# Optimization experiments

Hardware: AMD Instinct MI355X
Metric: run time of the kernel (lower is better)

The kernel has to match this reference:

```python
import jax, jax.numpy as jnp
import numpy as np

N_NODES = 100000
N_EDGES = 3200000
N_GRAPHS = 256
HIDDEN = 64
F_IN = 9
GRAPH_INPUTS = 4


def setup_inputs() -> dict:
    key = jax.random.key(0)
    ks = jax.random.split(key, 20)
    x = jax.random.normal(ks[0], (N_NODES, F_IN), dtype=jnp.float32)
    edge_index = jax.random.randint(ks[1], (2, N_EDGES), 0, N_NODES)
    batch = jnp.sort(jax.random.randint(ks[2], (N_NODES,), 0, N_GRAPHS))
    batch = batch.at[0].set(0).at[-1].set(N_GRAPHS - 1)
    u = jax.random.normal(ks[3], (N_GRAPHS, GRAPH_INPUTS), dtype=jnp.float32)

    def lin(k, fi, fo):
        k1, k2 = jax.random.split(k)
        s = 1.0 / np.sqrt(fi)
        W = jax.random.uniform(k1, (fi, fo), minval=-s, maxval=s, dtype=jnp.float32)
        b = jax.random.uniform(k2, (fo,), minval=-s, maxval=s, dtype=jnp.float32)
        return W, b

    W1, b1 = lin(ks[4], F_IN, HIDDEN)
    W2, b2 = lin(ks[5], HIDDEN, HIDDEN)
    W3, b3 = lin(ks[6], HIDDEN, HIDDEN)
    A1, c1 = lin(ks[7], HIDDEN + GRAPH_INPUTS, 50)
    A2, c2 = lin(ks[8], 50, 30)
    A3, c3 = lin(ks[9], 30, 20)
    A4, c4 = lin(ks[10], 20, 5)
    A5, c5 = lin(ks[11], 5, 1)
    return dict(x=x, edge_index=edge_index, batch=batch, u=u,
                W1=W1, b1=b1, W2=W2, b2=b2, W3=W3, b3=b3,
                A1=A1, c1=c1, A2=A2, c2=c2, A3=A3, c3=c3,
                A4=A4, c4=c4, A5=A5, c5=c5)


def reference(x, edge_index, batch, u,
              W1, b1, W2, b2, W3, b3,
              A1, c1, A2, c2, A3, c3, A4, c4, A5, c5):
    N = x.shape[0]
    loops = jnp.arange(N, dtype=edge_index.dtype)
    src = jnp.concatenate([edge_index[0], loops])  # self-loops appended (PyG GCNConv default)
    dst = jnp.concatenate([edge_index[1], loops])
    deg = jax.ops.segment_sum(jnp.ones_like(dst, dtype=x.dtype), dst, num_segments=N)
    dinv = jax.lax.rsqrt(jnp.maximum(deg, 1.0))  # deg >= 1 due to self-loops
    norm = dinv[src] * dinv[dst]  # symmetric normalization

    def conv(h, W, b):
        h = h @ W
        msg = h[src] * norm[:, None]          # gather + scale
        return jax.ops.segment_sum(msg, dst, num_segments=N) + b  # scatter-add

    h = jax.nn.relu(conv(x, W1, b1))
    h = jax.nn.relu(conv(h, W2, b2))
    h = jax.nn.relu(conv(h, W3, b3))

    G = u.shape[0]
    sums = jax.ops.segment_sum(h, batch, num_segments=G)
    cnt = jax.ops.segment_sum(jnp.ones((N,), x.dtype), batch, num_segments=G)
    pooled = sums / jnp.maximum(cnt, 1.0)[:, None]  # global_mean_pool
    # dropout p=0.2 is identity at inference (training=False)
    z = jnp.concatenate([pooled, u], axis=1)
    z = jax.nn.relu(z @ A1 + c1)
    z = jax.nn.relu(z @ A2 + c2)
    z = jax.nn.relu(z @ A3 + c3)
    z = jax.nn.relu(z @ A4 + c4)
    z = jax.nn.relu(z @ A5 + c5)
    return z
```

## Files before the change

kernel.cpp:

```cpp
#include <hip/hip_runtime.h>

#define H 64
#define BNODE_SHIFT 8
#define BNODES 256
#define CHUNK 4096
#define EPT 16

static __device__ __forceinline__ float b2f(ushort b) {
    return __uint_as_float(((unsigned int)b) << 16);
}
static __device__ __forceinline__ ushort f2b(float f) {
    unsigned int u = __float_as_uint(f);
    return (ushort)((u + 0x7FFF + ((u >> 16) & 1)) >> 16);
}

__global__ void zero_i32(int* p, int n) {
    int i = blockIdx.x * blockDim.x + threadIdx.x;
    if (i < n) p[i] = 0;
}

__global__ void bucket_hist(const int* __restrict__ dst, int E,
                            int* __restrict__ bcounts, int nbuck) {
    __shared__ int hist[512];
    for (int i = threadIdx.x; i < nbuck; i += blockDim.x) hist[i] = 0;
    __syncthreads();
    for (int e = blockIdx.x * blockDim.x + threadIdx.x; e < E; e += gridDim.x * blockDim.x)
        atomicAdd(&hist[dst[e] >> BNODE_SHIFT], 1);
    __syncthreads();
    for (int i = threadIdx.x; i < nbuck; i += blockDim.x) {
        int v = hist[i];
        if (v) atomicAdd(&bcounts[i], v);
    }
}

__global__ void bucket_scan(const int* __restrict__ bcounts, int* __restrict__ boff,
                            int* __restrict__ bcur, int* __restrict__ rowstart,
                            int nbuck, int E, int N) {
    __shared__ int t[1024];
    int tid = threadIdx.x;
    int v = (tid < nbuck) ? bcounts[tid] : 0;
    t[tid] = v;
    __syncthreads();
    for (int off = 1; off < 1024; off <<= 1) {
        int x = (tid >= off) ? t[tid - off] : 0;
        __syncthreads();
        t[tid] += x;
        __syncthreads();
    }
    if (tid < nbuck) {
        int o = t[tid] - v;
        boff[tid] = o;
        bcur[tid * 16] = o;
    }
    if (tid == 0) { boff[nbuck] = E; rowstart[N] = E; }
}

__global__ void edge_sort_scatter(const int* __restrict__ src, const int* __restrict__ dst,
                                  int E, int nbuck,
                                  int* __restrict__ bcur, int* __restrict__ pairs4) {
    __shared__ int hist[392];
    __shared__ int bstart[393];
    __shared__ int cur[392];
    __shared__ int gbase[392];
    __shared__ int wsum[256];
    __shared__ int packed[CHUNK];
    __shared__ int gpos[CHUNK];

    int t = threadIdx.x;
    int chunkBase = blockIdx.x * CHUNK;

    for (int i = t; i < nbuck; i += 256) hist[i] = 0;
    __syncthreads();
#pragma unroll
    for (int k = 0; k < EPT; ++k) {
        int e = chunkBase + t + k * 256;
        if (e < E) atomicAdd(&hist[dst[e] >> BNODE_SHIFT], 1);
    }
    __syncthreads();

    int a0 = (2 * t < nbuck) ? hist[2 * t] : 0;
    int a1 = (2 * t + 1 < nbuck) ? hist[2 * t + 1] : 0;
    int s2 = a0 + a1;
    wsum[t] = s2;
    __syncthreads();
    for (int off = 1; off < 256; off <<= 1) {
        int x = (t >= off) ? wsum[t - off] : 0;
        __syncthreads();
        wsum[t] += x;
        __syncthreads();
    }
    int base = wsum[t] - s2;
    if (2 * t < nbuck)     bstart[2 * t] = base;
    if (2 * t + 1 < nbuck) bstart[2 * t + 1] = base + a0;
    if (t == 255) bstart[nbuck] = wsum[255];
    __syncthreads();

    for (int b = t; b < nbuck; b += 256) {
        int cnt = bstart[b + 1] - bstart[b];
        gbase[b] = cnt ? (atomicAdd(&bcur[b * 16], cnt) - bstart[b]) : 0;
        cur[b] = bstart[b];
    }
    __syncthreads();

    #pragma unroll
    for (int k = 0; k < EPT; ++k) {
        int e = chunkBase + t + k * 256;
        if (e < E) {
            int d = dst[e];
            int b = d >> BNODE_SHIFT;
            int pos = atomicAdd(&cur[b], 1);
            packed[pos] = src[e] | ((d & (BNODES - 1)) << 20);
            gpos[pos] = gbase[b] + pos;
        }
    }
    __syncthreads();

    int nloc = bstart[nbuck];
    for (int j = t; j < nloc; j += 256)
        pairs4[gpos[j]] = packed[j];
}

__global__ void bucket_build(const int* __restrict__ pairs4, const int* __restrict__ boff,
                             int* __restrict__ col, int* __restrict__ rowstart,
                             float* __restrict__ dinv, int N) {
    __shared__ int hist[BNODES];
    __shared__ int cur[BNODES];
    int b = blockIdx.x;
    int lo = boff[b], hi = boff[b + 1];
    int node0 = b << BNODE_SHIFT;
    int tid = threadIdx.x;
    hist[tid] = 0;
    __syncthreads();
    for (int e = lo + tid; e < hi; e += 256)
        atomicAdd(&hist[(pairs4[e] >> 20) & (BNODES - 1)], 1);
    __syncthreads();
    int v = hist[tid];
    cur[tid] = v;
    __syncthreads();
    for (int off = 1; off < BNODES; off <<= 1) {
        int x = (tid >= off) ? cur[tid - off] : 0;
        __syncthreads();
        cur[tid] += x;
        __syncthreads();
    }
    {
        int ex = cur[tid] - v;
        int node = node0 + tid;
        if (node < N) {
            rowstart[node] = lo + ex;
            dinv[node] = rsqrtf((float)(v + 1));
        }
        cur[tid] = ex;
    }
    __syncthreads();
    for (int e = lo + tid; e < hi; e += 256) {
        int pr = pairs4[e];
        int p = atomicAdd(&cur[(pr >> 20) & (BNODES - 1)], 1);
        col[lo + p] = pr & 0xFFFFF;
    }
}

__global__ void graph_bounds(const int* __restrict__ batch, int* __restrict__ nodestart,
                             int N, int G) {
    int i = blockIdx.x * blockDim.x + threadIdx.x;
    if (i >= N) return;
    int b = batch[i];
    int bp = (i == 0) ? -1 : batch[i - 1];
    for (int g = bp + 1; g <= b; ++g) nodestart[g] = i;
    if (i == N - 1) nodestart[G] = N;
}

__global__ void pool_mean(const float* __restrict__ h, const int* __restrict__ nodestart,
                          float* __restrict__ pooled, int G) {
    int g = blockIdx.x;
    int lo = nodestart[g], hi = nodestart[g + 1];
    int f = threadIdx.x & 63, w = threadIdx.x >> 6;
    float acc = 0.f;
    for (int n = lo + w; n < hi; n += 4) acc += h[(size_t)n * H + f];
    __shared__ float red[4][64];
    red[w][f] = acc;
    __syncthreads();
    if (w == 0) {
        float s = red[0][f] + red[1][f] + red[2][f] + red[3][f];
        float c = (float)(hi - lo);
        pooled[g * H + f] = s / fmaxf(c, 1.f);
    }
}

__global__ void prep_xb(const float* __restrict__ x, const float* __restrict__ dinv,
                        ushort* __restrict__ xb, int N) {
    int i = blockIdx.x * blockDim.x + threadIdx.x;
    if (i >= N * 16) return;
    int n = i >> 4, k = i & 15;
    xb[i] = (k < 9) ? f2b(x[n * 9 + k] * dinv[n]) : (ushort)0;
}

__global__ void conv1_fused(const ushort* __restrict__ xb, const float* __restrict__ dinv,
                            const int* __restrict__ rowstart,
                            const int* __restrict__ col, const float* __restrict__ W1,
                            const float* __restrict__ b1, float* __restrict__ out, int N) {
    int gtid = blockIdx.x * blockDim.x + threadIdx.x;
    int i = __builtin_amdgcn_readfirstlane(gtid >> 6);
    int lane = threadIdx.x & 63;
    int f16 = lane & 15, grp = lane >> 4;
    if (i >= N) return;
    float di = dinv[i];
    float sv = b2f(xb[(size_t)i * 16 + f16]);
    float acc = 0.f;
    int s = rowstart[i], e = rowstart[i + 1];
    for (int base = s; base < e; base += 64) {
        int cnt = e - base;
        if (cnt > 64) cnt = 64;
        int idx = 0;
        if (lane < cnt) idx = col[base + lane];
        for (int j = 0; j < cnt; j += 8) {
            int j0 = j + grp, j1 = j + 4 + grp;
            int s0 = __shfl(idx, j0);
            int s1 = __shfl(idx, j1 & 63);
            float v0 = (j0 < cnt) ? b2f(xb[(size_t)s0 * 16 + f16]) : 0.f;
            float v1 = (j1 < cnt) ? b2f(xb[(size_t)s1 * 16 + f16]) : 0.f;
            acc += v0 + v1;
        }
    }
    acc += __shfl_xor(acc, 16);
    acc += __shfl_xor(acc, 32);
    float aggf = di * (acc + sv);

    float o = b1[lane];
#pragma unroll
    for (int k = 0; k < 9; ++k) {
        float ak = __shfl(aggf, k);
        o = fmaf(ak, W1[k * H + lane], o);
    }
    out[(size_t)i * H + lane] = fmaxf(o, 0.f);
}

__global__ void lin_h(const float* __restrict__ h, const float* __restrict__ W,
                      const float* __restrict__ dinv, ushort* __restrict__ out, int N) {
    __shared__ float Ws[H * H];
    __shared__ float hs[16 * H];
    int tid = threadIdx.x;
    int node0 = blockIdx.x * 16;
    for (int idx = tid; idx < H * H; idx += 256) Ws[idx] = W[idx];
    for (int idx = tid; idx < 16 * H; idx += 256) {
        int n = node0 + (idx >> 6);
        hs[idx] = (n < N) ? h[n * H + (idx & 63)] : 0.f;
    }
    __syncthreads();
    int nlb = tid >> 6, f = tid & 63;
    float a0 = 0.f, a1 = 0.f, a2 = 0.f, a3 = 0.f;
#pragma unroll 8
    for (int k = 0; k < H; ++k) {
        float w = Ws[k * H + f];
        a0 += hs[(nlb) * H + k] * w;
        a1 += hs[(nlb + 4) * H + k] * w;
        a2 += hs[(nlb + 8) * H + k] * w;
        a3 += hs[(nlb + 12) * H + k] * w;
    }
    int n;
    n = node0 + nlb;      if (n < N) out[n * H + f] = f2b(a0 * dinv[n]);
    n = node0 + nlb + 4;  if (n < N) out[n * H + f] = f2b(a1 * dinv[n]);
    n = node0 + nlb + 8;  if (n < N) out[n * H + f] = f2b(a2 * dinv[n]);
    n = node0 + nlb + 12; if (n < N) out[n * H + f] = f2b(a3 * dinv[n]);
}

__global__ void aggregate_b(const ushort* __restrict__ hb, const float* __restrict__ dinv,
                            const int* __restrict__ rowstart,
                            const int* __restrict__ col, const float* __restrict__ bias,
                            float* __restrict__ out, int N) {
    int gtid = blockIdx.x * blockDim.x + threadIdx.x;
    int i = __builtin_amdgcn_readfirstlane(gtid >> 6);
    int f = threadIdx.x & 63;
    if (i >= N) return;
    float acc = b2f(hb[(size_t)i * H + f]);
    int s = rowstart[i], e = rowstart[i + 1];
    int p = s;
    for (; p + 8 <= e; p += 8) {
        int i0 = __builtin_amdgcn_readfirstlane(col[p + 0]);
        int i1 = __builtin_amdgcn_readfirstlane(col[p + 1]);
        int i2 = __builtin_amdgcn_readfirstlane(col[p + 2]);
        int i3 = __builtin_amdgcn_readfirstlane(col[p + 3]);
        int i4 = __builtin_amdgcn_readfirstlane(col[p + 4]);
        int i5 = __builtin_amdgcn_readfirstlane(col[p + 5]);
        int i6 = __builtin_amdgcn_readfirstlane(col[p + 6]);
        int i7 = __builtin_amdgcn_readfirstlane(col[p + 7]);
        float v0 = b2f(hb[(size_t)i0 * H + f]);
        float v1 = b2f(hb[(size_t)i1 * H + f]);
        float v2 = b2f(hb[(size_t)i2 * H + f]);
        float v3 = b2f(hb[(size_t)i3 * H + f]);
        float v4 = b2f(hb[(size_t)i4 * H + f]);
        float v5 = b2f(hb[(size_t)i5 * H + f]);
        float v6 = b2f(hb[(size_t)i6 * H + f]);
        float v7 = b2f(hb[(size_t)i7 * H + f]);
        acc += ((v0 + v1) + (v2 + v3)) + ((v4 + v5) + (v6 + v7));
    }
    for (; p < e; ++p) {
        int s0 = __builtin_amdgcn_readfirstlane(col[p]);
        acc += b2f(hb[(size_t)s0 * H + f]);
    }
    out[(size_t)i * H + f] = fmaxf(bias[f] + dinv[i] * acc, 0.f);
}

__global__ void mlp(const float* __restrict__ pooled, const float* __restrict__ u,
                    const float* __restrict__ A1, const float* __restrict__ c1,
                    const float* __restrict__ A2, const float* __restrict__ c2,
                    const float* __restrict__ A3, const float* __restrict__ c3,
                    const float* __restrict__ A4, const float* __restrict__ c4,
                    const float* __restrict__ A5, const float* __restrict__ c5,
                    float* __restrict__ out, int G) {
    int wid = (blockIdx.x * blockDim.x + threadIdx.x) >> 6;
    int lane = threadIdx.x & 63;
    if (wid >= G) return;
    int g = wid;

    float zreg = pooled[g * H + lane];
    float u0 = u[g * 4 + 0], u1 = u[g * 4 + 1], u2 = u[g * 4 + 2], u3 = u[g * 4 + 3];

    float acc = (lane < 50) ? c1[lane] : 0.f;
#pragma unroll
    for (int k = 0; k < 64; ++k) {
        float zk = __shfl(zreg, k);
        float w = (lane < 50) ? A1[k * 50 + lane] : 0.f;
        acc = fmaf(zk, w, acc);
    }
    {
        float w;
        w = (lane < 50) ? A1[64 * 50 + lane] : 0.f; acc = fmaf(u0, w, acc);
        w = (lane < 50) ? A1[65 * 50 + lane] : 0.f; acc = fmaf(u1, w, acc);
        w = (lane < 50) ? A1[66 * 50 + lane] : 0.f; acc = fmaf(u2, w, acc);
        w = (lane < 50) ? A1[67 * 50 + lane] : 0.f; acc = fmaf(u3, w, acc);
    }
    float z1v = fmaxf(acc, 0.f);

    acc = (lane < 30) ? c2[lane] : 0.f;
#pragma unroll
    for (int k = 0; k < 50; ++k) {
        float zk = __shfl(z1v, k);
        float w = (lane < 30) ? A2[k * 30 + lane] : 0.f;
        acc = fmaf(zk, w, acc);
    }
    float z2v = fmaxf(acc, 0.f);

    acc = (lane < 20) ? c3[lane] : 0.f;
#pragma unroll
    for (int k = 0; k < 30; ++k) {
        float zk = __shfl(z2v, k);
        float w = (lane < 20) ? A3[k * 20 + lane] : 0.f;
        acc = fmaf(zk, w, acc);
    }
    float z3v = fmaxf(acc, 0.f);

    acc = (lane < 5) ? c4[lane] : 0.f;
#pragma unroll
    for (int k = 0; k < 20; ++k) {
        float zk = __shfl(z3v, k);
        float w = (lane < 5) ? A4[k * 5 + lane] : 0.f;
        acc = fmaf(zk, w, acc);
    }
    float z4v = fmaxf(acc, 0.f);

    acc = c5[0];
#pragma unroll
    for (int k = 0; k < 5; ++k) {
        float zk = __shfl(z4v, k);
        acc = fmaf(zk, A5[k], acc);
    }
    if (lane == 0) out[g] = fmaxf(acc, 0.f);
}

extern "C" void kernel_launch(void* const* d_in, const int* in_sizes, int n_in,
                              void* d_out, int out_size, void* d_ws, size_t ws_size,
                              hipStream_t stream) {
    const float* x     = (const float*)d_in[0];
    const int*   edge  = (const int*)d_in[1];
    const int*   batch = (const int*)d_in[2];
    const float* u     = (const float*)d_in[3];
    const float* W1 = (const float*)d_in[4];  const float* b1 = (const float*)d_in[5];
    const float* W2 = (const float*)d_in[6];  const float* b2 = (const float*)d_in[7];
    const float* W3 = (const float*)d_in[8];  const float* b3 = (const float*)d_in[9];
    const float* A1 = (const float*)d_in[10]; const float* c1 = (const float*)d_in[11];
    const float* A2 = (const float*)d_in[12]; const float* c2 = (const float*)d_in[13];
    const float* A3 = (const float*)d_in[14]; const float* c3 = (const float*)d_in[15];
    const float* A4 = (const float*)d_in[16]; const float* c4 = (const float*)d_in[17];
    const float* A5 = (const float*)d_in[18]; const float* c5 = (const float*)d_in[19];

    const int N = in_sizes[2];
    const int E = in_sizes[1] / 2;
    const int G = in_sizes[3] / 4;
    const int* src = edge;
    const int* dst = edge + E;
    const int nbuck = (N + BNODES - 1) >> BNODE_SHIFT;

    char* ws = (char*)d_ws;
    size_t off = 0;
    auto alloc = [&](size_t bytes) -> void* {
        void* p = ws + off;
        off = (off + bytes + 255) & ~(size_t)255;
        return p;
    };
    ushort* hb       = (ushort*)alloc((size_t)N * H * 2);
    float*  h        = (float*)alloc((size_t)N * H * 4);
    int*    col      = (int*)alloc((size_t)E * 4);
    ushort* xb       = (ushort*)alloc((size_t)N * 16 * 2);
    int*    rowstart = (int*)alloc((size_t)(N + 1) * 4);
    float*  dinv     = (float*)alloc((size_t)N * 4);
    int*    bcounts  = (int*)alloc((size_t)nbuck * 4);
    int*    boff     = (int*)alloc((size_t)(nbuck + 1) * 4);
    int*    bcur     = (int*)alloc((size_t)nbuck * 64);
    int*    nodestart= (int*)alloc((size_t)(G + 1) * 4);
    float*  pooled   = (float*)alloc((size_t)G * H * 4);
    int*    pairs4   = (int*)hb;

    const int nbN   = (N + 255) / 256;
    const int nbAgg = (N + 3) / 4;
    const int nchunks = (E + CHUNK - 1) / CHUNK;

    zero_i32<<<(nbuck + 255) / 256, 256, 0, stream>>>(bcounts, nbuck);
    bucket_hist<<<256, 256, 0, stream>>>(dst, E, bcounts, nbuck);
    bucket_scan<<<1, 1024, 0, stream>>>(bcounts, boff, bcur, rowstart, nbuck, E, N);
    edge_sort_scatter<<<nchunks, 256, 0, stream>>>(src, dst, E, nbuck, bcur, pairs4);
    bucket_build<<<nbuck, 256, 0, stream>>>(pairs4, boff, col, rowstart, dinv, N);
    graph_bounds<<<nbN, 256, 0, stream>>>(batch, nodestart, N, G);

    prep_xb<<<(N * 16 + 255) / 256, 256, 0, stream>>>(x, dinv, xb, N);
    conv1_fused<<<nbAgg, 256, 0, stream>>>(xb, dinv, rowstart, col, W1, b1, h, N);
    lin_h<<<(N + 15) / 16, 256, 0, stream>>>(h, W2, dinv, hb, N);
    aggregate_b<<<nbAgg, 256, 0, stream>>>(hb, dinv, rowstart, col, b2, h, N);
    lin_h<<<(N + 15) / 16, 256, 0, stream>>>(h, W3, dinv, hb, N);
    aggregate_b<<<nbAgg, 256, 0, stream>>>(hb, dinv, rowstart, col, b3, h, N);

    pool_mean<<<G, 256, 0, stream>>>(h, nodestart, pooled, G);
    mlp<<<(G * 64 + 255) / 256, 256, 0, stream>>>(pooled, u, A1, c1, A2, c2, A3, c3,
                                                  A4, c4, A5, c5, (float*)d_out, G);
}
```

Baseline: 390.5 us.

## Split hidden features into two half-width planes and aggregate each in separate passes

lin_h now writes the bf16 hidden features as two separate 32-wide planes instead of one 64-wide array. Aggregation runs as two launches, one per half. Within each launch a wave covers two neighbours per load, one per 32-lane half, and the halves are combined with a cross-lane shuffle. The aim is to shrink the gather working set per pass (N*64 bytes) so it fits better in cache, improving hit rates on random neighbour reads, at the cost of reading the CSR column indices twice and launching extra kernels. Output stores are also made nontemporal.

```diff
diff --git a/kernel.cpp b/kernel.cpp
--- a/kernel.cpp
+++ b/kernel.cpp
@@ -13,6 +13,7 @@
     unsigned int u = __float_as_uint(f);
     return (ushort)((u + 0x7FFF + ((u >> 16) & 1)) >> 16);
 }
+#define RFL(x) __builtin_amdgcn_readfirstlane(x)
 
 __global__ void zero_i32(int* p, int n) {
     int i = blockIdx.x * blockDim.x + threadIdx.x;
@@ -200,7 +201,7 @@
                             const int* __restrict__ col, const float* __restrict__ W1,
                             const float* __restrict__ b1, float* __restrict__ out, int N) {
     int gtid = blockIdx.x * blockDim.x + threadIdx.x;
-    int i = __builtin_amdgcn_readfirstlane(gtid >> 6);
+    int i = RFL(gtid >> 6);
     int lane = threadIdx.x & 63;
     int f16 = lane & 15, grp = lane >> 4;
     if (i >= N) return;
@@ -236,7 +237,8 @@
 }
 
 __global__ void lin_h(const float* __restrict__ h, const float* __restrict__ W,
-                      const float* __restrict__ dinv, ushort* __restrict__ out, int N) {
+                      const float* __restrict__ dinv,
+                      ushort* __restrict__ out0, ushort* __restrict__ out1, int N) {
     __shared__ float Ws[H * H];
     __shared__ float hs[16 * H];
     int tid = threadIdx.x;
@@ -257,48 +259,71 @@
         a2 += hs[(nlb + 8) * H + k] * w;
         a3 += hs[(nlb + 12) * H + k] * w;
     }
+    ushort* op = (f < 32) ? out0 : out1;
+    int fo = f & 31;
     int n;
-    n = node0 + nlb;      if (n < N) out[n * H + f] = f2b(a0 * dinv[n]);
-    n = node0 + nlb + 4;  if (n < N) out[n * H + f] = f2b(a1 * dinv[n]);
-    n = node0 + nlb + 8;  if (n < N) out[n * H + f] = f2b(a2 * dinv[n]);
-    n = node0 + nlb + 12; if (n < N) out[n * H + f] = f2b(a3 * dinv[n]);
-}
-
-__global__ void aggregate_b(const ushort* __restrict__ hb, const float* __restrict__ dinv,
+    n = node0 + nlb;      if (n < N) op[(size_t)n * 32 + fo] = f2b(a0 * dinv[n]);
+    n = node0 + nlb + 4;  if (n < N) op[(size_t)n * 32 + fo] = f2b(a1 * dinv[n]);
+    n = node0 + nlb + 8;  if (n < N) op[(size_t)n * 32 + fo] = f2b(a2 * dinv[n]);
+    n = node0 + nlb + 12; if (n < N) op[(size_t)n * 32 + fo] = f2b(a3 * dinv[n]);
+}
+
+template <int HALF>
+__global__ void aggregate_h(const ushort* __restrict__ hp, const float* __restrict__ dinv,
                             const int* __restrict__ rowstart,
                             const int* __restrict__ col, const float* __restrict__ bias,
                             float* __restrict__ out, int N) {
     int gtid = blockIdx.x * blockDim.x + threadIdx.x;
-    int i = __builtin_amdgcn_readfirstlane(gtid >> 6);
-    int f = threadIdx.x & 63;
+    int i = RFL(gtid >> 6);
+    int lane = threadIdx.x & 63;
+    int f = lane & 31, pr = lane >> 5;
     if (i >= N) return;
-    float acc = b2f(hb[(size_t)i * H + f]);
+    float self = b2f(hp[(size_t)i * 32 + f]);
+    float acc = 0.f;
     int s = rowstart[i], e = rowstart[i + 1];
     int p = s;
-    for (; p + 8 <= e; p += 8) {
-        int i0 = __builtin_amdgcn_readfirstlane(col[p + 0]);
-        int i1 = __builtin_amdgcn_readfirstlane(col[p + 1]);
-        int i2 = __builtin_amdgcn_readfirstlane(col[p + 2]);
-        int i3 = __builtin_amdgcn_readfirstlane(col[p + 3]);
-        int i4 = __builtin_amdgcn_readfirstlane(col[p + 4]);
-        int i5 = __builtin_amdgcn_readfirstlane(col[p + 5]);
-        int i6 = __builtin_amdgcn_readfirstlane(col[p + 6]);
-        int i7 = __builtin_amdgcn_readfirstlane(col[p + 7]);
-        float v0 = b2f(hb[(size_t)i0 * H + f]);
-        float v1 = b2f(hb[(size_t)i1 * H + f]);
-        float v2 = b2f(hb[(size_t)i2 * H + f]);
-        float v3 = b2f(hb[(size_t)i3 * H + f]);
-        float v4 = b2f(hb[(size_t)i4 * H + f]);
-        float v5 = b2f(hb[(size_t)i5 * H + f]);
-        float v6 = b2f(hb[(size_t)i6 * H + f]);
-        float v7 = b2f(hb[(size_t)i7 * H + f]);
+    for (; p + 16 <= e; p += 16) {
+        int a0 = RFL(col[p + 0]),  a1 = RFL(col[p + 1]);
+        int a2 = RFL(col[p + 2]),  a3 = RFL(col[p + 3]);
+        int a4 = RFL(col[p + 4]),  a5 = RFL(col[p + 5]);
+        int a6 = RFL(col[p + 6]),  a7 = RFL(col[p + 7]);
+        int a8 = RFL(col[p + 8]),  a9 = RFL(col[p + 9]);
+        int aA = RFL(col[p + 10]), aB = RFL(col[p + 11]);
+        int aC = RFL(col[p + 12]), aD = RFL(col[p + 13]);
+        int aE = RFL(col[p + 14]), aF = RFL(col[p + 15]);
+        int s0 = pr ? a1 : a0;
+        int s1 = pr ? a3 : a2;
+        int s2 = pr ? a5 : a4;
+        int s3 = pr ? a7 : a6;
+        int s4 = pr ? a9 : a8;
+        int s5 = pr ? aB : aA;
+        int s6 = pr ? aD : aC;
+        int s7 = pr ? aF : aE;
+        float v0 = b2f(hp[(size_t)s0 * 32 + f]);
+        float v1 = b2f(hp[(size_t)s1 * 32 + f]);
+        float v2 = b2f(hp[(size_t)s2 * 32 + f]);
+        float v3 = b2f(hp[(size_t)s3 * 32 + f]);
+        float v4 = b2f(hp[(size_t)s4 * 32 + f]);
+        float v5 = b2f(hp[(size_t)s5 * 32 + f]);
+        float v6 = b2f(hp[(size_t)s6 * 32 + f]);
+        float v7 = b2f(hp[(size_t)s7 * 32 + f]);
         acc += ((v0 + v1) + (v2 + v3)) + ((v4 + v5) + (v6 + v7));
     }
-    for (; p < e; ++p) {
-        int s0 = __builtin_amdgcn_readfirstlane(col[p]);
-        acc += b2f(hb[(size_t)s0 * H + f]);
-    }
-    out[(size_t)i * H + f] = fmaxf(bias[f] + dinv[i] * acc, 0.f);
+    for (; p + 2 <= e; p += 2) {
+        int a0 = RFL(col[p]), a1 = RFL(col[p + 1]);
+        int s0 = pr ? a1 : a0;
+        acc += b2f(hp[(size_t)s0 * 32 + f]);
+    }
+    if (p < e) {
+        int a0 = RFL(col[p]);
+        float v = b2f(hp[(size_t)a0 * 32 + f]);
+        if (pr == 0) acc += v;
+    }
+    acc += __shfl_xor(acc, 32);
+    if (pr == 0) {
+        float r = fmaxf(bias[HALF * 32 + f] + dinv[i] * (acc + self), 0.f);
+        __builtin_nontemporal_store(r, &out[(size_t)i * H + HALF * 32 + f]);
+    }
 }
 
 __global__ void mlp(const float* __restrict__ pooled, const float* __restrict__ u,
@@ -398,7 +423,8 @@
         off = (off + bytes + 255) & ~(size_t)255;
         return p;
     };
-    ushort* hb       = (ushort*)alloc((size_t)N * H * 2);
+    ushort* hb0      = (ushort*)alloc((size_t)N * 32 * 2);
+    ushort* hb1      = (ushort*)alloc((size_t)N * 32 * 2);
     float*  h        = (float*)alloc((size_t)N * H * 4);
     int*    col      = (int*)alloc((size_t)E * 4);
     ushort* xb       = (ushort*)alloc((size_t)N * 16 * 2);
@@ -409,7 +435,7 @@
     int*    bcur     = (int*)alloc((size_t)nbuck * 64);
     int*    nodestart= (int*)alloc((size_t)(G + 1) * 4);
     float*  pooled   = (float*)alloc((size_t)G * H * 4);
-    int*    pairs4   = (int*)hb;
+    int*    pairs4   = (int*)hb0;
 
     const int nbN   = (N + 255) / 256;
     const int nbAgg = (N + 3) / 4;
@@ -424,10 +450,12 @@
 
     prep_xb<<<(N * 16 + 255) / 256, 256, 0, stream>>>(x, dinv, xb, N);
     conv1_fused<<<nbAgg, 256, 0, stream>>>(xb, dinv, rowstart, col, W1, b1, h, N);
-    lin_h<<<(N + 15) / 16, 256, 0, stream>>>(h, W2, dinv, hb, N);
-    aggregate_b<<<nbAgg, 256, 0, stream>>>(hb, dinv, rowstart, col, b2, h, N);
-    lin_h<<<(N + 15) / 16, 256, 0, stream>>>(h, W3, dinv, hb, N);
-    aggregate_b<<<nbAgg, 256, 0, stream>>>(hb, dinv, rowstart, col, b3, h, N);
+    lin_h<<<(N + 15) / 16, 256, 0, stream>>>(h, W2, dinv, hb0, hb1, N);
+    aggregate_h<0><<<nbAgg, 256, 0, stream>>>(hb0, dinv, rowstart, col, b2, h, N);
+    aggregate_h<1><<<nbAgg, 256, 0, stream>>>(hb1, dinv, rowstart, col, b2, h, N);
+    lin_h<<<(N + 15) / 16, 256, 0, stream>>>(h, W3, dinv, hb0, hb1, N);
+    aggregate_h<0><<<nbAgg, 256, 0, stream>>>(hb0, dinv, rowstart, col, b3, h, N);
+    aggregate_h<1><<<nbAgg, 256, 0, stream>>>(hb1, dinv, rowstart, col, b3, h, N);
 
     pool_mean<<<G, 256, 0, stream>>>(h, nodestart, pooled, G);
     mlp<<<(G * 64 + 255) / 256, 256, 0, stream>>>(pooled, u, A1, c1, A2, c2, A3, c3,
```

Result: slower. 490.3 us (+25.6%).

## Reorder GCN layers to aggregate-then-transform and fuse mean-pool via atomics

Applied to the files above, without the earlier changes.

Uses the identity A(hW) = (Ah)W so each of layers 2 and 3 becomes one kernel: gather and aggregate the bf16 previous activations, then apply the 64x64 weight from shared memory within the wave. Conv1 and layer 2 now write pre-scaled bf16 outputs directly, which removes the fp32 intermediate buffer and the separate lin_h kernels. Layer 3 accumulates straight into per-graph pool sums with atomicAdd, and mlp divides by the node count, so pool_mean is gone. In exchange, every block now stages the full weight matrix in LDS, and there is atomic contention on 256×64 pool entries plus a float-atomic summation order that is not deterministic.

```diff
diff --git a/kernel.cpp b/kernel.cpp
--- a/kernel.cpp
+++ b/kernel.cpp
@@ -13,10 +13,15 @@
     unsigned int u = __float_as_uint(f);
     return (ushort)((u + 0x7FFF + ((u >> 16) & 1)) >> 16);
 }
+#define RFL(x) __builtin_amdgcn_readfirstlane(x)
 
 __global__ void zero_i32(int* p, int n) {
     int i = blockIdx.x * blockDim.x + threadIdx.x;
     if (i < n) p[i] = 0;
+}
+__global__ void zero_f32(float* p, int n) {
+    int i = blockIdx.x * blockDim.x + threadIdx.x;
+    if (i < n) p[i] = 0.f;
 }
 
 __global__ void bucket_hist(const int* __restrict__ dst, int E,
@@ -170,23 +175,6 @@
     if (i == N - 1) nodestart[G] = N;
 }
 
-__global__ void pool_mean(const float* __restrict__ h, const int* __restrict__ nodestart,
-                          float* __restrict__ pooled, int G) {
-    int g = blockIdx.x;
-    int lo = nodestart[g], hi = nodestart[g + 1];
-    int f = threadIdx.x & 63, w = threadIdx.x >> 6;
-    float acc = 0.f;
-    for (int n = lo + w; n < hi; n += 4) acc += h[(size_t)n * H + f];
-    __shared__ float red[4][64];
-    red[w][f] = acc;
-    __syncthreads();
-    if (w == 0) {
-        float s = red[0][f] + red[1][f] + red[2][f] + red[3][f];
-        float c = (float)(hi - lo);
-        pooled[g * H + f] = s / fmaxf(c, 1.f);
-    }
-}
-
 __global__ void prep_xb(const float* __restrict__ x, const float* __restrict__ dinv,
                         ushort* __restrict__ xb, int N) {
     int i = blockIdx.x * blockDim.x + threadIdx.x;
@@ -198,9 +186,9 @@
 __global__ void conv1_fused(const ushort* __restrict__ xb, const float* __restrict__ dinv,
                             const int* __restrict__ rowstart,
                             const int* __restrict__ col, const float* __restrict__ W1,
-                            const float* __restrict__ b1, float* __restrict__ out, int N) {
+                            const float* __restrict__ b1, ushort* __restrict__ outb, int N) {
     int gtid = blockIdx.x * blockDim.x + threadIdx.x;
-    int i = __builtin_amdgcn_readfirstlane(gtid >> 6);
+    int i = RFL(gtid >> 6);
     int lane = threadIdx.x & 63;
     int f16 = lane & 15, grp = lane >> 4;
     if (i >= N) return;
@@ -232,58 +220,41 @@
         float ak = __shfl(aggf, k);
         o = fmaf(ak, W1[k * H + lane], o);
     }
-    out[(size_t)i * H + lane] = fmaxf(o, 0.f);
-}
-
-__global__ void lin_h(const float* __restrict__ h, const float* __restrict__ W,
-                      const float* __restrict__ dinv, ushort* __restrict__ out, int N) {
+    outb[(size_t)i * H + lane] = f2b(fmaxf(o, 0.f) * di);
+}
+
+template <int MODE>
+__global__ void agg_mm(const ushort* __restrict__ hb, const float* __restrict__ dinv,
+                       const int* __restrict__ rowstart, const int* __restrict__ col,
+                       const float* __restrict__ W, const float* __restrict__ bias,
+                       ushort* __restrict__ outb, float* __restrict__ pool,
+                       const int* __restrict__ batch, int N) {
     __shared__ float Ws[H * H];
-    __shared__ float hs[16 * H];
-    int tid = threadIdx.x;
-    int node0 = blockIdx.x * 16;
-    for (int idx = tid; idx < H * H; idx += 256) Ws[idx] = W[idx];
-    for (int idx = tid; idx < 16 * H; idx += 256) {
-        int n = node0 + (idx >> 6);
-        hs[idx] = (n < N) ? h[n * H + (idx & 63)] : 0.f;
-    }
-    __syncthreads();
-    int nlb = tid >> 6, f = tid & 63;
-    float a0 = 0.f, a1 = 0.f, a2 = 0.f, a3 = 0.f;
-#pragma unroll 8
-    for (int k = 0; k < H; ++k) {
-        float w = Ws[k * H + f];
-        a0 += hs[(nlb) * H + k] * w;
-        a1 += hs[(nlb + 4) * H + k] * w;
-        a2 += hs[(nlb + 8) * H + k] * w;
-        a3 += hs[(nlb + 12) * H + k] * w;
-    }
-    int n;
-    n = node0 + nlb;      if (n < N) out[n * H + f] = f2b(a0 * dinv[n]);
-    n = node0 + nlb + 4;  if (n < N) out[n * H + f] = f2b(a1 * dinv[n]);
-    n = node0 + nlb + 8;  if (n < N) out[n * H + f] = f2b(a2 * dinv[n]);
-    n = node0 + nlb + 12; if (n < N) out[n * H + f] = f2b(a3 * dinv[n]);
-}
-
-__global__ void aggregate_b(const ushort* __restrict__ hb, const float* __restrict__ dinv,
-                            const int* __restrict__ rowstart,
-                            const int* __restrict__ col, const float* __restrict__ bias,
-                            float* __restrict__ out, int N) {
-    int gtid = blockIdx.x * blockDim.x + threadIdx.x;
-    int i = __builtin_amdgcn_readfirstlane(gtid >> 6);
-    int f = threadIdx.x & 63;
-    if (i >= N) return;
-    float acc = b2f(hb[(size_t)i * H + f]);
-    int s = rowstart[i], e = rowstart[i + 1];
+    int t = threadIdx.x;
+    for (int idx = t; idx < H * H; idx += 256) Ws[idx] = W[idx];
+
+    int gtid = blockIdx.x * blockDim.x + t;
+    int i = RFL(gtid >> 6);
+    int f = t & 63;
+    bool active = (i < N);
+    float acc = 0.f, di = 0.f;
+    int s = 0, e = 0;
+    if (active) {
+        di = dinv[i];
+        acc = b2f(hb[(size_t)i * H + f]);
+        s = rowstart[i];
+        e = rowstart[i + 1];
+    }
     int p = s;
     for (; p + 8 <= e; p += 8) {
-        int i0 = __builtin_amdgcn_readfirstlane(col[p + 0]);
-        int i1 = __builtin_amdgcn_readfirstlane(col[p + 1]);
-        int i2 = __builtin_amdgcn_readfirstlane(col[p + 2]);
-        int i3 = __builtin_amdgcn_readfirstlane(col[p + 3]);
-        int i4 = __builtin_amdgcn_readfirstlane(col[p + 4]);
-        int i5 = __builtin_amdgcn_readfirstlane(col[p + 5]);
-        int i6 = __builtin_amdgcn_readfirstlane(col[p + 6]);
-        int i7 = __builtin_amdgcn_readfirstlane(col[p + 7]);
+        int i0 = RFL(col[p + 0]);
+        int i1 = RFL(col[p + 1]);
+        int i2 = RFL(col[p + 2]);
+        int i3 = RFL(col[p + 3]);
+        int i4 = RFL(col[p + 4]);
+        int i5 = RFL(col[p + 5]);
+        int i6 = RFL(col[p + 6]);
+        int i7 = RFL(col[p + 7]);
         float v0 = b2f(hb[(size_t)i0 * H + f]);
         float v1 = b2f(hb[(size_t)i1 * H + f]);
         float v2 = b2f(hb[(size_t)i2 * H + f]);
@@ -295,13 +266,29 @@
         acc += ((v0 + v1) + (v2 + v3)) + ((v4 + v5) + (v6 + v7));
     }
     for (; p < e; ++p) {
-        int s0 = __builtin_amdgcn_readfirstlane(col[p]);
+        int s0 = RFL(col[p]);
         acc += b2f(hb[(size_t)s0 * H + f]);
     }
-    out[(size_t)i * H + f] = fmaxf(bias[f] + dinv[i] * acc, 0.f);
-}
-
-__global__ void mlp(const float* __restrict__ pooled, const float* __restrict__ u,
+    __syncthreads();
+    if (!active) return;
+
+    float aggv = di * acc;
+    float o = bias[f];
+#pragma unroll
+    for (int k = 0; k < H; ++k) {
+        float ak = __shfl(aggv, k);
+        o = fmaf(ak, Ws[k * H + f], o);
+    }
+    o = fmaxf(o, 0.f);
+    if (MODE == 0) {
+        outb[(size_t)i * H + f] = f2b(o * di);
+    } else {
+        atomicAdd(&pool[(size_t)batch[i] * H + f], o);
+    }
+}
+
+__global__ void mlp(const float* __restrict__ pool, const int* __restrict__ nodestart,
+                    const float* __restrict__ u,
                     const float* __restrict__ A1, const float* __restrict__ c1,
                     const float* __restrict__ A2, const float* __restrict__ c2,
                     const float* __restrict__ A3, const float* __restrict__ c3,
@@ -313,7 +300,9 @@
     if (wid >= G) return;
     int g = wid;
 
-    float zreg = pooled[g * H + lane];
+    float cntf = (float)(nodestart[g + 1] - nodestart[g]);
+    float inv = 1.f / fmaxf(cntf, 1.f);
+    float zreg = pool[g * H + lane] * inv;
     float u0 = u[g * 4 + 0], u1 = u[g * 4 + 1], u2 = u[g * 4 + 2], u3 = u[g * 4 + 3];
 
     float acc = (lane < 50) ? c1[lane] : 0.f;
@@ -398,8 +387,8 @@
         off = (off + bytes + 255) & ~(size_t)255;
         return p;
     };
-    ushort* hb       = (ushort*)alloc((size_t)N * H * 2);
-    float*  h        = (float*)alloc((size_t)N * H * 4);
+    ushort* hb_a     = (ushort*)alloc((size_t)N * H * 2);
+    ushort* hb_b     = (ushort*)alloc((size_t)N * H * 2);
     int*    col      = (int*)alloc((size_t)E * 4);
     ushort* xb       = (ushort*)alloc((size_t)N * 16 * 2);
     int*    rowstart = (int*)alloc((size_t)(N + 1) * 4);
@@ -408,14 +397,15 @@
     int*    boff     = (int*)alloc((size_t)(nbuck + 1) * 4);
     int*    bcur     = (int*)alloc((size_t)nbuck * 64);
     int*    nodestart= (int*)alloc((size_t)(G + 1) * 4);
-    float*  pooled   = (float*)alloc((size_t)G * H * 4);
-    int*    pairs4   = (int*)hb;
+    float*  pool     = (float*)alloc((size_t)G * H * 4);
+    int*    pairs4   = (int*)hb_a;
 
     const int nbN   = (N + 255) / 256;
     const int nbAgg = (N + 3) / 4;
     const int nchunks = (E + CHUNK - 1) / CHUNK;
 
     zero_i32<<<(nbuck + 255) / 256, 256, 0, stream>>>(bcounts, nbuck);
+    zero_f32<<<(G * H + 255) / 256, 256, 0, stream>>>(pool, G * H);
     bucket_hist<<<256, 256, 0, stream>>>(dst, E, bcounts, nbuck);
     bucket_scan<<<1, 1024, 0, stream>>>(bcounts, boff, bcur, rowstart, nbuck, E, N);
     edge_sort_scatter<<<nchunks, 256, 0, stream>>>(src, dst, E, nbuck, bcur, pairs4);
@@ -423,13 +413,13 @@
     graph_bounds<<<nbN, 256, 0, stream>>>(batch, nodestart, N, G);
 
     prep_xb<<<(N * 16 + 255) / 256, 256, 0, stream>>>(x, dinv, xb, N);
-    conv1_fused<<<nbAgg, 256, 0, stream>>>(xb, dinv, rowstart, col, W1, b1, h, N);
-    lin_h<<<(N + 15) / 16, 256, 0, stream>>>(h, W2, dinv, hb, N);
-    aggregate_b<<<nbAgg, 256, 0, stream>>>(hb, dinv, rowstart, col, b2, h, N);
-    lin_h<<<(N + 15) / 16, 256, 0, stream>>>(h, W3, dinv, hb, N);
-    aggregate_b<<<nbAgg, 256, 0, stream>>>(hb, dinv, rowstart, col, b3, h, N);
-
-    pool_mean<<<G, 256, 0, stream>>>(h, nodestart, pooled, G);
-    mlp<<<(G * 64 + 255) / 256, 256, 0, stream>>>(pooled, u, A1, c1, A2, c2, A3, c3,
-                                                  A4, c4, A5, c5, (float*)d_out, G);
-}
+    conv1_fused<<<nbAgg, 256, 0, stream>>>(xb, dinv, rowstart, col, W1, b1, hb_a, N);
+    agg_mm<0><<<nbAgg, 256, 0, stream>>>(hb_a, dinv, rowstart, col, W2, b2,
+                                         hb_b, nullptr, nullptr, N);
+    agg_mm<1><<<nbAgg, 256, 0, stream>>>(hb_b, dinv, rowstart, col, W3, b3,
+                                         nullptr, pool, batch, N);
+
+    mlp<<<(G * 64 + 255) / 256, 256, 0, stream>>>(pool, nodestart, u, A1, c1, A2, c2,
+                                                  A3, c3, A4, c4, A5, c5,
+                                                  (float*)d_out, G);
+}
```

New measurement: 501.5 us. 1.28x slower.

## Store intermediate node features in bf16, add nontemporal hints, enlarge lin_h tile

Applied to the files above, without the earlier changes.

The fp32 intermediate activation buffer between conv, lin and aggregate stages is replaced with a bf16 buffer, which halves the bytes written and read for h. Edge-index loads and output stores now use nontemporal hints so the streaming col array does less to evict the gathered feature table from cache. lin_h now processes 32 nodes per block with 8 accumulators instead of 16 nodes with 4. This adds extra bf16 rounding of the post-ReLU activations, and the larger tile raises register and LDS use per block.

```diff
diff --git a/kernel.cpp b/kernel.cpp
--- a/kernel.cpp
+++ b/kernel.cpp
@@ -13,6 +13,7 @@
     unsigned int u = __float_as_uint(f);
     return (ushort)((u + 0x7FFF + ((u >> 16) & 1)) >> 16);
 }
+#define RFL(x) __builtin_amdgcn_readfirstlane(x)
 
 __global__ void zero_i32(int* p, int n) {
     int i = blockIdx.x * blockDim.x + threadIdx.x;
@@ -170,13 +171,13 @@
     if (i == N - 1) nodestart[G] = N;
 }
 
-__global__ void pool_mean(const float* __restrict__ h, const int* __restrict__ nodestart,
+__global__ void pool_mean(const ushort* __restrict__ h, const int* __restrict__ nodestart,
                           float* __restrict__ pooled, int G) {
     int g = blockIdx.x;
     int lo = nodestart[g], hi = nodestart[g + 1];
     int f = threadIdx.x & 63, w = threadIdx.x >> 6;
     float acc = 0.f;
-    for (int n = lo + w; n < hi; n += 4) acc += h[(size_t)n * H + f];
+    for (int n = lo + w; n < hi; n += 4) acc += b2f(h[(size_t)n * H + f]);
     __shared__ float red[4][64];
     red[w][f] = acc;
     __syncthreads();
@@ -198,9 +199,9 @@
 __global__ void conv1_fused(const ushort* __restrict__ xb, const float* __restrict__ dinv,
                             const int* __restrict__ rowstart,
                             const int* __restrict__ col, const float* __restrict__ W1,
-                            const float* __restrict__ b1, float* __restrict__ out, int N) {
+                            const float* __restrict__ b1, ushort* __restrict__ out, int N) {
     int gtid = blockIdx.x * blockDim.x + threadIdx.x;
-    int i = __builtin_amdgcn_readfirstlane(gtid >> 6);
+    int i = RFL(gtid >> 6);
     int lane = threadIdx.x & 63;
     int f16 = lane & 15, grp = lane >> 4;
     if (i >= N) return;
@@ -212,7 +213,7 @@
         int cnt = e - base;
         if (cnt > 64) cnt = 64;
         int idx = 0;
-        if (lane < cnt) idx = col[base + lane];
+        if (lane < cnt) idx = __builtin_nontemporal_load(&col[base + lane]);
         for (int j = 0; j < cnt; j += 8) {
             int j0 = j + grp, j1 = j + 4 + grp;
             int s0 = __shfl(idx, j0);
@@ -232,58 +233,60 @@
         float ak = __shfl(aggf, k);
         o = fmaf(ak, W1[k * H + lane], o);
     }
-    out[(size_t)i * H + lane] = fmaxf(o, 0.f);
-}
-
-__global__ void lin_h(const float* __restrict__ h, const float* __restrict__ W,
+    __builtin_nontemporal_store(f2b(fmaxf(o, 0.f)), &out[(size_t)i * H + lane]);
+}
+
+__global__ void lin_h(const ushort* __restrict__ h, const float* __restrict__ W,
                       const float* __restrict__ dinv, ushort* __restrict__ out, int N) {
     __shared__ float Ws[H * H];
-    __shared__ float hs[16 * H];
+    __shared__ float hs[32 * H];
     int tid = threadIdx.x;
-    int node0 = blockIdx.x * 16;
+    int node0 = blockIdx.x * 32;
     for (int idx = tid; idx < H * H; idx += 256) Ws[idx] = W[idx];
-    for (int idx = tid; idx < 16 * H; idx += 256) {
+    for (int idx = tid; idx < 32 * H; idx += 256) {
         int n = node0 + (idx >> 6);
-        hs[idx] = (n < N) ? h[n * H + (idx & 63)] : 0.f;
+        hs[idx] = (n < N) ? b2f(h[(size_t)n * H + (idx & 63)]) : 0.f;
     }
     __syncthreads();
     int nlb = tid >> 6, f = tid & 63;
-    float a0 = 0.f, a1 = 0.f, a2 = 0.f, a3 = 0.f;
+    float a[8];
+#pragma unroll
+    for (int j = 0; j < 8; ++j) a[j] = 0.f;
 #pragma unroll 8
     for (int k = 0; k < H; ++k) {
         float w = Ws[k * H + f];
-        a0 += hs[(nlb) * H + k] * w;
-        a1 += hs[(nlb + 4) * H + k] * w;
-        a2 += hs[(nlb + 8) * H + k] * w;
-        a3 += hs[(nlb + 12) * H + k] * w;
-    }
-    int n;
-    n = node0 + nlb;      if (n < N) out[n * H + f] = f2b(a0 * dinv[n]);
-    n = node0 + nlb + 4;  if (n < N) out[n * H + f] = f2b(a1 * dinv[n]);
-    n = node0 + nlb + 8;  if (n < N) out[n * H + f] = f2b(a2 * dinv[n]);
-    n = node0 + nlb + 12; if (n < N) out[n * H + f] = f2b(a3 * dinv[n]);
+#pragma unroll
+        for (int j = 0; j < 8; ++j)
+            a[j] = fmaf(hs[(nlb + 4 * j) * H + k], w, a[j]);
+    }
+#pragma unroll
+    for (int j = 0; j < 8; ++j) {
+        int n = node0 + nlb + 4 * j;
+        if (n < N)
+            __builtin_nontemporal_store(f2b(a[j] * dinv[n]), &out[(size_t)n * H + f]);
+    }
 }
 
 __global__ void aggregate_b(const ushort* __restrict__ hb, const float* __restrict__ dinv,
                             const int* __restrict__ rowstart,
                             const int* __restrict__ col, const float* __restrict__ bias,
-                            float* __restrict__ out, int N) {
+                            ushort* __restrict__ out, int N) {
     int gtid = blockIdx.x * blockDim.x + threadIdx.x;
-    int i = __builtin_amdgcn_readfirstlane(gtid >> 6);
+    int i = RFL(gtid >> 6);
     int f = threadIdx.x & 63;
     if (i >= N) return;
     float acc = b2f(hb[(size_t)i * H + f]);
     int s = rowstart[i], e = rowstart[i + 1];
     int p = s;
     for (; p + 8 <= e; p += 8) {
-        int i0 = __builtin_amdgcn_readfirstlane(col[p + 0]);
-        int i1 = __builtin_amdgcn_readfirstlane(col[p + 1]);
-        int i2 = __builtin_amdgcn_readfirstlane(col[p + 2]);
-        int i3 = __builtin_amdgcn_readfirstlane(col[p + 3]);
-        int i4 = __builtin_amdgcn_readfirstlane(col[p + 4]);
-        int i5 = __builtin_amdgcn_readfirstlane(col[p + 5]);
-        int i6 = __builtin_amdgcn_readfirstlane(col[p + 6]);
-        int i7 = __builtin_amdgcn_readfirstlane(col[p + 7]);
+        int i0 = RFL(__builtin_nontemporal_load(&col[p + 0]));
+        int i1 = RFL(__builtin_nontemporal_load(&col[p + 1]));
+        int i2 = RFL(__builtin_nontemporal_load(&col[p + 2]));
+        int i3 = RFL(__builtin_nontemporal_load(&col[p + 3]));
+        int i4 = RFL(__builtin_nontemporal_load(&col[p + 4]));
+        int i5 = RFL(__builtin_nontemporal_load(&col[p + 5]));
+        int i6 = RFL(__builtin_nontemporal_load(&col[p + 6]));
+        int i7 = RFL(__builtin_nontemporal_load(&col[p + 7]));
         float v0 = b2f(hb[(size_t)i0 * H + f]);
         float v1 = b2f(hb[(size_t)i1 * H + f]);
         float v2 = b2f(hb[(size_t)i2 * H + f]);
@@ -295,10 +298,11 @@
         acc += ((v0 + v1) + (v2 + v3)) + ((v4 + v5) + (v6 + v7));
     }
     for (; p < e; ++p) {
-        int s0 = __builtin_amdgcn_readfirstlane(col[p]);
+        int s0 = RFL(__builtin_nontemporal_load(&col[p]));
         acc += b2f(hb[(size_t)s0 * H + f]);
     }
-    out[(size_t)i * H + f] = fmaxf(bias[f] + dinv[i] * acc, 0.f);
+    float r = fmaxf(bias[f] + dinv[i] * acc, 0.f);
+    __builtin_nontemporal_store(f2b(r), &out[(size_t)i * H + f]);
 }
 
 __global__ void mlp(const float* __restrict__ pooled, const float* __restrict__ u,
@@ -399,7 +403,7 @@
         return p;
     };
     ushort* hb       = (ushort*)alloc((size_t)N * H * 2);
-    float*  h        = (float*)alloc((size_t)N * H * 4);
+    ushort* hc       = (ushort*)alloc((size_t)N * H * 2);
     int*    col      = (int*)alloc((size_t)E * 4);
     ushort* xb       = (ushort*)alloc((size_t)N * 16 * 2);
     int*    rowstart = (int*)alloc((size_t)(N + 1) * 4);
@@ -423,13 +427,13 @@
     graph_bounds<<<nbN, 256, 0, stream>>>(batch, nodestart, N, G);
 
     prep_xb<<<(N * 16 + 255) / 256, 256, 0, stream>>>(x, dinv, xb, N);
-    conv1_fused<<<nbAgg, 256, 0, stream>>>(xb, dinv, rowstart, col, W1, b1, h, N);
-    lin_h<<<(N + 15) / 16, 256, 0, stream>>>(h, W2, dinv, hb, N);
-    aggregate_b<<<nbAgg, 256, 0, stream>>>(hb, dinv, rowstart, col, b2, h, N);
-    lin_h<<<(N + 15) / 16, 256, 0, stream>>>(h, W3, dinv, hb, N);
-    aggregate_b<<<nbAgg, 256, 0, stream>>>(hb, dinv, rowstart, col, b3, h, N);
-
-    pool_mean<<<G, 256, 0, stream>>>(h, nodestart, pooled, G);
+    conv1_fused<<<nbAgg, 256, 0, stream>>>(xb, dinv, rowstart, col, W1, b1, hc, N);
+    lin_h<<<(N + 31) / 32, 256, 0, stream>>>(hc, W2, dinv, hb, N);
+    aggregate_b<<<nbAgg, 256, 0, stream>>>(hb, dinv, rowstart, col, b2, hc, N);
+    lin_h<<<(N + 31) / 32, 256, 0, stream>>>(hc, W3, dinv, hb, N);
+    aggregate_b<<<nbAgg, 256, 0, stream>>>(hb, dinv, rowstart, col, b3, hc, N);
+
+    pool_mean<<<G, 256, 0, stream>>>(hc, nodestart, pooled, G);
     mlp<<<(G * 64 + 255) / 256, 256, 0, stream>>>(pooled, u, A1, c1, A2, c2, A3, c3,
                                                   A4, c4, A5, c5, (float*)d_out, G);
 }
```

New measurement: 422.4 us. +8.2%, slower.
